# Kernel optimization log

Measured on AMD Instinct MI355X. Metric: run time of the kernel, lower is better.

The kernel has to match this reference:

```python
import jax, jax.numpy as jnp
import numpy as np

M_SQRT1_2 = 0.7071067811865476
P_DROP = 0.1  # activation_dropout


def setup_inputs() -> dict:
    key = jax.random.key(0)
    k1, k2, k3, k4 = jax.random.split(key, 4)
    N, FFN, EMB = 8192, 4096, 1024
    x = jax.random.normal(k1, (N, FFN), dtype=jnp.float16)
    weight = (jax.random.normal(k2, (EMB, FFN), dtype=jnp.float32) * (1.0 / np.sqrt(FFN))).astype(jnp.float16)
    bias = jax.random.normal(k3, (EMB,), dtype=jnp.float16)
    mask = jax.random.uniform(k4, (N, FFN)) >= P_DROP  # keep mask (bool)
    return {"x": x, "weight": weight, "bias": bias, "mask": mask}


def reference(x, weight, bias, mask):
    # GELU computed in fp32, cast back to fp16 (matches the custom IR)
    xf = x.astype(jnp.float32)
    g = (0.5 * xf * (1.0 + jax.lax.erf(xf * M_SQRT1_2))).astype(jnp.float16)
    # dropout: mask then scale by 1/(1-p) in fp16
    scale = jnp.float16(1.0 / (1.0 - P_DROP))
    h = g * mask.astype(jnp.float16) * scale  # [N, FFN]
    # y[N0, N2] = sum_N1 h[N0, N1] * weight[N2, N1] + bias[N2]
    y = jnp.einsum('nf,ef->ne', h, weight) + bias[None, :]
    return y
```

## Files before the change

kernel.cpp:

```cpp
#include <hip/hip_runtime.h>
#include <stdint.h>

typedef uint32_t u32;
typedef uint16_t u16;

static constexpr int M_DIM = 8192;
static constexpr int N_DIM = 1024;
static constexpr int K_DIM = 4096;

static constexpr int BM = 256;
static constexpr int BN = 128;
static constexpr int BK = 64;
static constexpr int KT64 = K_DIM / BK;
static constexpr int K_TILES32 = K_DIM / 32;
static constexpr int MB_TILES = M_DIM / 16;
static constexpr int NB_TILES = N_DIM / 16;

static constexpr size_t FRAG_U16 = 512;
static constexpr size_t HT_BYTES = (size_t)MB_TILES * K_TILES32 * FRAG_U16 * 2;
static constexpr size_t WT_BYTES = (size_t)NB_TILES * K_TILES32 * FRAG_U16 * 2;
static constexpr size_t WS_NEEDED = HT_BYTES + WT_BYTES;

typedef __attribute__((ext_vector_type(8))) _Float16 half8;
typedef __attribute__((ext_vector_type(4))) float f32x4;

__device__ __forceinline__ u32 pack2(float a, float b) {
  union { _Float16 h[2]; u32 u; } p;
  p.h[0] = (_Float16)a;
  p.h[1] = (_Float16)b;
  return p.u;
}

__device__ __forceinline__ float gelu_drop(float x, u32 keep) {
  float ax = fabsf(x);
  float z  = ax * 0.70710678f;
  float t  = __builtin_amdgcn_rcpf(fmaf(0.3275911f, z, 1.0f));
  float poly = fmaf(fmaf(fmaf(fmaf(1.061405429f, t, -1.453152027f),
                              t, 1.421413741f),
                         t, -0.284496736f),
                    t, 0.254829592f) * t;
  float e   = exp2f(z * z * -1.44269504f);
  float erf = fmaf(-poly, e, 1.0f);
  float g   = 0.5f * x * (1.0f + copysignf(erf, x));
  return keep ? g * 1.1111112f : 0.0f;
}

__device__ __forceinline__ void async_cp16(const void* g, void* l) {
  __builtin_amdgcn_global_load_lds((__attribute__((address_space(1))) u32*)g,
                                   (__attribute__((address_space(3))) u32*)l,
                                   16, 0, 0);
}

static constexpr int H_PAIRS = MB_TILES * (K_TILES32 / 2);
static constexpr int W_PAIRS = NB_TILES * (K_TILES32 / 2);
static constexpr int PACK_BLOCKS = (H_PAIRS + W_PAIRS) / 4;

__global__ __launch_bounds__(256)
void pack_kernel(const float* __restrict__ X, const int* __restrict__ Mask,
                 const float* __restrict__ W, u16* __restrict__ Ht, u16* __restrict__ Wt) {
  const int l     = threadIdx.x & 63;
  const int pi    = blockIdx.x * 4 + (threadIdx.x >> 6);
  const int row16 = l & 15;
  const int kof   = (l >> 4) << 4;

  const int fsub = kof >> 5;
  const int q0   = (kof & 31) >> 3;

  if (pi < H_PAIRS) {
    const int mb = pi >> 6, kp = pi & 63;
    const size_t src = (size_t)(mb * 16 + row16) * K_DIM + kp * 64 + kof;
    const float* xp = X    + src;
    const int*   mp = Mask + src;
    float4 x0 = *(const float4*)(xp + 0);
    float4 x1 = *(const float4*)(xp + 4);
    float4 x2 = *(const float4*)(xp + 8);
    float4 x3 = *(const float4*)(xp + 12);
    uint4  m0 = *(const uint4*)(mp + 0);
    uint4  m1 = *(const uint4*)(mp + 4);
    uint4  m2 = *(const uint4*)(mp + 8);
    uint4  m3 = *(const uint4*)(mp + 12);
    u32 o0 = pack2(gelu_drop(x0.x, m0.x), gelu_drop(x0.y, m0.y));
    u32 o1 = pack2(gelu_drop(x0.z, m0.z), gelu_drop(x0.w, m0.w));
    u32 o2 = pack2(gelu_drop(x1.x, m1.x), gelu_drop(x1.y, m1.y));
    u32 o3 = pack2(gelu_drop(x1.z, m1.z), gelu_drop(x1.w, m1.w));
    u32 o4 = pack2(gelu_drop(x2.x, m2.x), gelu_drop(x2.y, m2.y));
    u32 o5 = pack2(gelu_drop(x2.z, m2.z), gelu_drop(x2.w, m2.w));
    u32 o6 = pack2(gelu_drop(x3.x, m3.x), gelu_drop(x3.y, m3.y));
    u32 o7 = pack2(gelu_drop(x3.z, m3.z), gelu_drop(x3.w, m3.w));
    const int f = kp * 2 + fsub;
    u16* dst = Ht + (size_t)(mb * 128 + f) * FRAG_U16 + (size_t)(row16 + 16 * q0) * 8;
    *(uint4*)(dst)       = make_uint4(o0, o1, o2, o3);
    *(uint4*)(dst + 128) = make_uint4(o4, o5, o6, o7);
  } else {
    const int pj = pi - H_PAIRS;
    const int nb = pj >> 6, kp = pj & 63;
    const float* wp = W + (size_t)(nb * 16 + row16) * K_DIM + kp * 64 + kof;
    float4 w0 = *(const float4*)(wp + 0);
    float4 w1 = *(const float4*)(wp + 4);
    float4 w2 = *(const float4*)(wp + 8);
    float4 w3 = *(const float4*)(wp + 12);
    const int f = kp * 2 + fsub;
    u16* dst = Wt + (size_t)(nb * 128 + f) * FRAG_U16 + (size_t)(row16 + 16 * q0) * 8;
    *(uint4*)(dst)       = make_uint4(pack2(w0.x, w0.y), pack2(w0.z, w0.w),
                                      pack2(w1.x, w1.y), pack2(w1.z, w1.w));
    *(uint4*)(dst + 128) = make_uint4(pack2(w2.x, w2.y), pack2(w2.z, w2.w),
                                      pack2(w3.x, w3.y), pack2(w3.z, w3.w));
  }
}

__global__ __launch_bounds__(512, 1)
void gemm_kernel(const u16* __restrict__ Ht, const u16* __restrict__ Wt,
                 const float* __restrict__ Bias, float* __restrict__ Out) {
  __shared__ __attribute__((aligned(16))) u16 Abuf[3][BM * BK];
  __shared__ __attribute__((aligned(16))) u16 Bbuf[3][BN * BK];

  const int tid  = threadIdx.x;
  const int lane = tid & 63;
  const int wv   = tid >> 6;
  const int wr   = wv >> 1;
  const int wc   = wv & 1;

  const int bm = blockIdx.x & 31;
  const int bn = blockIdx.x >> 5;
  const int m0 = bm * BM;
  const int n0 = bn * BN;

  const char* aG = (const char*)Ht;
  const char* bG = (const char*)Wt;
  size_t aOff[4], bOff[2];
#pragma unroll
  for (int p = 0; p < 4; ++p) {
    const int s = tid + 512 * p, f = s >> 6;
    aOff[p] = ((size_t)(bm * 16 + (f >> 1)) * K_TILES32 + (f & 1)) * 1024 + (size_t)(s & 63) * 16;
  }
#pragma unroll
  for (int p = 0; p < 2; ++p) {
    const int s = tid + 512 * p, f = s >> 6;
    bOff[p] = ((size_t)(bn * 8 + (f >> 1)) * K_TILES32 + (f & 1)) * 1024 + (size_t)(s & 63) * 16;
  }

  auto stageHalf = [&](int kt, int buf, int h) {
    const size_t ko = (size_t)kt * 2048;
    char* ad = (char*)Abuf[buf];
    char* bd = (char*)Bbuf[buf];
    if (h == 0) {
      async_cp16(aG + aOff[0] + ko, ad + (size_t)(tid)*16);
      async_cp16(aG + aOff[1] + ko, ad + (size_t)(tid + 512) * 16);
      async_cp16(bG + bOff[0] + ko, bd + (size_t)(tid)*16);
    } else {
      async_cp16(aG + aOff[2] + ko, ad + (size_t)(tid + 1024) * 16);
      async_cp16(aG + aOff[3] + ko, ad + (size_t)(tid + 1536) * 16);
      async_cp16(bG + bOff[1] + ko, bd + (size_t)(tid + 512) * 16);
    }
  };

  auto stageFull = [&](int kt, int buf) {
    stageHalf(kt, buf, 0);
    stageHalf(kt, buf, 1);
  };

  f32x4 acc[4][4];
#pragma unroll
  for (int i = 0; i < 4; ++i)
#pragma unroll
    for (int j = 0; j < 4; ++j)
      acc[i][j] = (f32x4){0.f, 0.f, 0.f, 0.f};

  auto phase = [&](int buf, int kk, int stKt, int stBuf, int h, int vm) {
    const char* ab = (const char*)Abuf[buf];
    const char* bb = (const char*)Bbuf[buf];
    half8 ar[4], br[4];
#pragma unroll
    for (int i = 0; i < 4; ++i)
      ar[i] = *(const half8*)(ab + (size_t)(((wr * 4 + i) * 2 + kk) * 64 + lane) * 16);
#pragma unroll
    for (int j = 0; j < 4; ++j)
      br[j] = *(const half8*)(bb + (size_t)(((wc * 4 + j) * 2 + kk) * 64 + lane) * 16);
    if (stKt >= 0) stageHalf(stKt, stBuf, h);
    if (vm == 6) asm volatile("s_waitcnt vmcnt(6)" ::: "memory");
    else if (vm == 0) asm volatile("s_waitcnt vmcnt(0)" ::: "memory");
    __builtin_amdgcn_s_barrier();
    asm volatile("s_waitcnt lgkmcnt(0)" ::: "memory");
    __builtin_amdgcn_sched_barrier(0);
    __builtin_amdgcn_s_setprio(1);
#pragma unroll
    for (int i = 0; i < 4; ++i)
#pragma unroll
      for (int j = 0; j < 4; ++j)
        acc[i][j] = __builtin_amdgcn_mfma_f32_16x16x32_f16(ar[i], br[j], acc[i][j], 0, 0, 0);
    __builtin_amdgcn_s_setprio(0);
    __builtin_amdgcn_sched_barrier(0);
    __builtin_amdgcn_s_barrier();
  };

  stageFull(0, 0);
  stageFull(1, 1);
  asm volatile("s_waitcnt vmcnt(6)" ::: "memory");
  __builtin_amdgcn_s_barrier();

#pragma unroll 1
  for (int kt = 0; kt < KT64; ++kt) {
    const int cur  = kt % 3;
    const bool st  = (kt + 2) < KT64;
    const int  sb  = (kt + 2) % 3;
    const int vm = st ? 6 : ((kt + 1) < KT64 ? 0 : -1);
    phase(cur, 0, st ? kt + 2 : -1, sb, 0, -1);
    phase(cur, 1, st ? kt + 2 : -1, sb, 1, vm);
  }

  const int fr = lane & 15;
  const int rq = (lane >> 4) << 2;
  float bv[4];
#pragma unroll
  for (int j = 0; j < 4; ++j)
    bv[j] = Bias[n0 + wc * 64 + j * 16 + fr];

#pragma unroll
  for (int i = 0; i < 4; ++i) {
    const int row0 = m0 + wr * 64 + i * 16 + rq;
#pragma unroll
    for (int j = 0; j < 4; ++j) {
      const int col = n0 + wc * 64 + j * 16 + fr;
#pragma unroll
      for (int r = 0; r < 4; ++r)
        Out[(size_t)(row0 + r) * N_DIM + col] = acc[i][j][r] + bv[j];
    }
  }
}

static constexpr int A_STRIDE = 40;

__global__ __launch_bounds__(256, 2)
void fused_fallback_kernel(const float* __restrict__ X, const float* __restrict__ W,
                           const float* __restrict__ Bias, const int* __restrict__ Mask,
                           float* __restrict__ Out) {
  __shared__ __attribute__((aligned(16))) _Float16 As[128 * A_STRIDE];
  __shared__ __attribute__((aligned(16))) _Float16 Bs[128 * 32];

  const int tid  = threadIdx.x;
  const int lane = tid & 63;
  const int wv   = tid >> 6;
  const int wr   = wv >> 1;
  const int wc   = wv & 1;
  const int bm = blockIdx.x & 63;
  const int bn = blockIdx.x >> 6;
  const int m0 = bm * 128;
  const int n0 = bn * 128;

  const int a_m = tid >> 1;
  const int a_k = (tid & 1) << 4;
  const float* xptr = X    + (size_t)(m0 + a_m) * K_DIM + a_k;
  const int*   mptr = Mask + (size_t)(m0 + a_m) * K_DIM + a_k;
  _Float16* a_lds = &As[a_m * A_STRIDE + a_k];

  const int i0 = tid, i1 = tid + 256;
  const float* wp0 = W + (size_t)(n0 + (i0 >> 2)) * K_DIM + ((i0 & 3) << 3);
  const float* wp1 = W + (size_t)(n0 + (i1 >> 2)) * K_DIM + ((i1 & 3) << 3);
  _Float16* bl0 = &Bs[i0 * 8];
  _Float16* bl1 = &Bs[i1 * 8];

  f32x4 acc[4][4];
#pragma unroll
  for (int i = 0; i < 4; ++i)
#pragma unroll
    for (int j = 0; j < 4; ++j)
      acc[i][j] = (f32x4){0.f, 0.f, 0.f, 0.f};

  float4 xf0 = *(const float4*)(xptr +  0);
  float4 xf1 = *(const float4*)(xptr +  4);
  float4 xf2 = *(const float4*)(xptr +  8);
  float4 xf3 = *(const float4*)(xptr + 12);
  uint4  mr0 = *(const uint4*)(mptr +  0);
  uint4  mr1 = *(const uint4*)(mptr +  4);
  uint4  mr2 = *(const uint4*)(mptr +  8);
  uint4  mr3 = *(const uint4*)(mptr + 12);
  float4 wf0 = *(const float4*)(wp0 + 0);
  float4 wf1 = *(const float4*)(wp0 + 4);
  float4 wf2 = *(const float4*)(wp1 + 0);
  float4 wf3 = *(const float4*)(wp1 + 4);

#pragma unroll 1
  for (int kt = 0; kt < 128; ++kt) {
    {
      float xs[16] = {xf0.x, xf0.y, xf0.z, xf0.w, xf1.x, xf1.y, xf1.z, xf1.w,
                      xf2.x, xf2.y, xf2.z, xf2.w, xf3.x, xf3.y, xf3.z, xf3.w};
      u32 mk[16]   = {mr0.x, mr0.y, mr0.z, mr0.w, mr1.x, mr1.y, mr1.z, mr1.w,
                      mr2.x, mr2.y, mr2.z, mr2.w, mr3.x, mr3.y, mr3.z, mr3.w};
      u32 ow[8];
#pragma unroll
      for (int e = 0; e < 8; ++e)
        ow[e] = pack2(gelu_drop(xs[2 * e], mk[2 * e]), gelu_drop(xs[2 * e + 1], mk[2 * e + 1]));
      ((uint4*)a_lds)[0] = make_uint4(ow[0], ow[1], ow[2], ow[3]);
      ((uint4*)a_lds)[1] = make_uint4(ow[4], ow[5], ow[6], ow[7]);
    }
    {
      *(uint4*)bl0 = make_uint4(pack2(wf0.x, wf0.y), pack2(wf0.z, wf0.w),
                                pack2(wf1.x, wf1.y), pack2(wf1.z, wf1.w));
      *(uint4*)bl1 = make_uint4(pack2(wf2.x, wf2.y), pack2(wf2.z, wf2.w),
                                pack2(wf3.x, wf3.y), pack2(wf3.z, wf3.w));
    }
    __syncthreads();

    if (kt + 1 < 128) {
      xptr += 32; mptr += 32; wp0 += 32; wp1 += 32;
      xf0 = *(const float4*)(xptr +  0);
      xf1 = *(const float4*)(xptr +  4);
      xf2 = *(const float4*)(xptr +  8);
      xf3 = *(const float4*)(xptr + 12);
      mr0 = *(const uint4*)(mptr +  0);
      mr1 = *(const uint4*)(mptr +  4);
      mr2 = *(const uint4*)(mptr +  8);
      mr3 = *(const uint4*)(mptr + 12);
      wf0 = *(const float4*)(wp0 + 0);
      wf1 = *(const float4*)(wp0 + 4);
      wf2 = *(const float4*)(wp1 + 0);
      wf3 = *(const float4*)(wp1 + 4);
    }

    {
      const int fr2 = lane & 15;
      const int fk2 = (lane >> 4) << 3;
      half8 ar[4], br[4];
#pragma unroll
      for (int i = 0; i < 4; ++i)
        ar[i] = *(const half8*)&As[(wr * 64 + i * 16 + fr2) * A_STRIDE + fk2];
#pragma unroll
      for (int j = 0; j < 4; ++j)
        br[j] = *(const half8*)&Bs[(wc * 64 + j * 16 + fr2) * 32 + fk2];
#pragma unroll
      for (int i = 0; i < 4; ++i)
#pragma unroll
        for (int j = 0; j < 4; ++j)
          acc[i][j] = __builtin_amdgcn_mfma_f32_16x16x32_f16(ar[i], br[j], acc[i][j], 0, 0, 0);
    }
    __syncthreads();
  }

  const int fr = lane & 15;
  const int rq = (lane >> 4) << 2;
  float bv[4];
#pragma unroll
  for (int j = 0; j < 4; ++j)
    bv[j] = Bias[n0 + wc * 64 + j * 16 + fr];
#pragma unroll
  for (int i = 0; i < 4; ++i) {
    const int row0 = m0 + wr * 64 + i * 16 + rq;
#pragma unroll
    for (int j = 0; j < 4; ++j) {
      const int col = n0 + wc * 64 + j * 16 + fr;
#pragma unroll
      for (int r = 0; r < 4; ++r)
        Out[(size_t)(row0 + r) * N_DIM + col] = acc[i][j][r] + bv[j];
    }
  }
}

extern "C" void kernel_launch(void* const* d_in, const int* in_sizes, int n_in,
                              void* d_out, int out_size, void* d_ws, size_t ws_size,
                              hipStream_t stream) {
  const float* X    = (const float*)d_in[0];
  const float* W    = (const float*)d_in[1];
  const float* Bias = (const float*)d_in[2];
  const int*   Mk   = (const int*)d_in[3];
  float* Out = (float*)d_out;

  if (ws_size >= WS_NEEDED) {
    u16* Ht = (u16*)d_ws;
    u16* Wt = (u16*)((char*)d_ws + HT_BYTES);
    pack_kernel<<<PACK_BLOCKS, 256, 0, stream>>>(X, Mk, W, Ht, Wt);
    gemm_kernel<<<(M_DIM / BM) * (N_DIM / BN), 512, 0, stream>>>(Ht, Wt, Bias, Out);
  } else {
    fused_fallback_kernel<<<64 * 8, 256, 0, stream>>>(X, W, Bias, Mk, Out);
  }
}
```

Baseline: 389.0 us.

## Fuse GELU-dropout into GEMM with full-N row tiles and streamed weights

Drops the separate pass that packed the activated input to workspace. GELU and dropout are now computed inside the GEMM: each block loads a 32-row slice of X and the mask, activates it, and writes it into swizzled LDS double buffers. Each block covers all 1024 output columns, while pre-packed fp16 weight fragments stream through a triple-buffered async LDS pipeline. This removes the fp16 H write and re-read, but every block re-streams the whole weight matrix (relying on L2), and each block does far less MFMA work per LDS B load.

```diff
diff --git a/kernel.cpp b/kernel.cpp
--- a/kernel.cpp
+++ b/kernel.cpp
@@ -8,18 +8,9 @@
 static constexpr int N_DIM = 1024;
 static constexpr int K_DIM = 4096;
 
-static constexpr int BM = 256;
-static constexpr int BN = 128;
-static constexpr int BK = 64;
-static constexpr int KT64 = K_DIM / BK;
-static constexpr int K_TILES32 = K_DIM / 32;
-static constexpr int MB_TILES = M_DIM / 16;
-static constexpr int NB_TILES = N_DIM / 16;
-
 static constexpr size_t FRAG_U16 = 512;
-static constexpr size_t HT_BYTES = (size_t)MB_TILES * K_TILES32 * FRAG_U16 * 2;
-static constexpr size_t WT_BYTES = (size_t)NB_TILES * K_TILES32 * FRAG_U16 * 2;
-static constexpr size_t WS_NEEDED = HT_BYTES + WT_BYTES;
+static constexpr size_t WT_BYTES = 64ull * 128 * FRAG_U16 * 2;
+static constexpr size_t WS_NEEDED = WT_BYTES;
 
 typedef __attribute__((ext_vector_type(8))) _Float16 half8;
 typedef __attribute__((ext_vector_type(4))) float f32x4;
@@ -51,179 +42,180 @@
                                    16, 0, 0);
 }
 
-static constexpr int H_PAIRS = MB_TILES * (K_TILES32 / 2);
-static constexpr int W_PAIRS = NB_TILES * (K_TILES32 / 2);
-static constexpr int PACK_BLOCKS = (H_PAIRS + W_PAIRS) / 4;
+__device__ __forceinline__ u32 aswz(u32 b) {
+  return b ^ (((b >> 8) & 3u) << 4) ^ (((b >> 10) & 1u) << 6);
+}
+
+static constexpr int W_PAIRS = 64 * 64;
+static constexpr int WPACK_BLOCKS = W_PAIRS / 4;
 
 __global__ __launch_bounds__(256)
-void pack_kernel(const float* __restrict__ X, const int* __restrict__ Mask,
-                 const float* __restrict__ W, u16* __restrict__ Ht, u16* __restrict__ Wt) {
+void wpack_kernel(const float* __restrict__ W, u16* __restrict__ Wt) {
   const int l     = threadIdx.x & 63;
-  const int pi    = blockIdx.x * 4 + (threadIdx.x >> 6);
+  const int pj    = blockIdx.x * 4 + (threadIdx.x >> 6);
   const int row16 = l & 15;
   const int kof   = (l >> 4) << 4;
-
-  const int fsub = kof >> 5;
-  const int q0   = (kof & 31) >> 3;
-
-  if (pi < H_PAIRS) {
-    const int mb = pi >> 6, kp = pi & 63;
-    const size_t src = (size_t)(mb * 16 + row16) * K_DIM + kp * 64 + kof;
-    const float* xp = X    + src;
-    const int*   mp = Mask + src;
-    float4 x0 = *(const float4*)(xp + 0);
-    float4 x1 = *(const float4*)(xp + 4);
-    float4 x2 = *(const float4*)(xp + 8);
-    float4 x3 = *(const float4*)(xp + 12);
-    uint4  m0 = *(const uint4*)(mp + 0);
-    uint4  m1 = *(const uint4*)(mp + 4);
-    uint4  m2 = *(const uint4*)(mp + 8);
-    uint4  m3 = *(const uint4*)(mp + 12);
-    u32 o0 = pack2(gelu_drop(x0.x, m0.x), gelu_drop(x0.y, m0.y));
-    u32 o1 = pack2(gelu_drop(x0.z, m0.z), gelu_drop(x0.w, m0.w));
-    u32 o2 = pack2(gelu_drop(x1.x, m1.x), gelu_drop(x1.y, m1.y));
-    u32 o3 = pack2(gelu_drop(x1.z, m1.z), gelu_drop(x1.w, m1.w));
-    u32 o4 = pack2(gelu_drop(x2.x, m2.x), gelu_drop(x2.y, m2.y));
-    u32 o5 = pack2(gelu_drop(x2.z, m2.z), gelu_drop(x2.w, m2.w));
-    u32 o6 = pack2(gelu_drop(x3.x, m3.x), gelu_drop(x3.y, m3.y));
-    u32 o7 = pack2(gelu_drop(x3.z, m3.z), gelu_drop(x3.w, m3.w));
-    const int f = kp * 2 + fsub;
-    u16* dst = Ht + (size_t)(mb * 128 + f) * FRAG_U16 + (size_t)(row16 + 16 * q0) * 8;
-    *(uint4*)(dst)       = make_uint4(o0, o1, o2, o3);
-    *(uint4*)(dst + 128) = make_uint4(o4, o5, o6, o7);
-  } else {
-    const int pj = pi - H_PAIRS;
-    const int nb = pj >> 6, kp = pj & 63;
-    const float* wp = W + (size_t)(nb * 16 + row16) * K_DIM + kp * 64 + kof;
-    float4 w0 = *(const float4*)(wp + 0);
-    float4 w1 = *(const float4*)(wp + 4);
-    float4 w2 = *(const float4*)(wp + 8);
-    float4 w3 = *(const float4*)(wp + 12);
-    const int f = kp * 2 + fsub;
-    u16* dst = Wt + (size_t)(nb * 128 + f) * FRAG_U16 + (size_t)(row16 + 16 * q0) * 8;
-    *(uint4*)(dst)       = make_uint4(pack2(w0.x, w0.y), pack2(w0.z, w0.w),
-                                      pack2(w1.x, w1.y), pack2(w1.z, w1.w));
-    *(uint4*)(dst + 128) = make_uint4(pack2(w2.x, w2.y), pack2(w2.z, w2.w),
-                                      pack2(w3.x, w3.y), pack2(w3.z, w3.w));
-  }
+  const int fsub  = kof >> 5;
+  const int q0    = (kof & 31) >> 3;
+
+  const int nb = pj >> 6, kp = pj & 63;
+  const float* wp = W + (size_t)(nb * 16 + row16) * K_DIM + kp * 64 + kof;
+  float4 w0 = *(const float4*)(wp + 0);
+  float4 w1 = *(const float4*)(wp + 4);
+  float4 w2 = *(const float4*)(wp + 8);
+  float4 w3 = *(const float4*)(wp + 12);
+  const int f = kp * 2 + fsub;
+  u16* dst = Wt + (size_t)(nb * 128 + f) * FRAG_U16 + (size_t)(row16 + 16 * q0) * 8;
+  *(uint4*)(dst)       = make_uint4(pack2(w0.x, w0.y), pack2(w0.z, w0.w),
+                                    pack2(w1.x, w1.y), pack2(w1.z, w1.w));
+  *(uint4*)(dst + 128) = make_uint4(pack2(w2.x, w2.y), pack2(w2.z, w2.w),
+                                    pack2(w3.x, w3.y), pack2(w3.z, w3.w));
 }
 
 __global__ __launch_bounds__(512, 1)
-void gemm_kernel(const u16* __restrict__ Ht, const u16* __restrict__ Wt,
-                 const float* __restrict__ Bias, float* __restrict__ Out) {
-  __shared__ __attribute__((aligned(16))) u16 Abuf[3][BM * BK];
-  __shared__ __attribute__((aligned(16))) u16 Bbuf[3][BN * BK];
+void fused_gemm_kernel(const float* __restrict__ X, const int* __restrict__ Mask,
+                       const u16* __restrict__ Wt, const float* __restrict__ Bias,
+                       float* __restrict__ Out) {
+  __shared__ __attribute__((aligned(16))) u16 Bbuf[3 * 16384];
+  __shared__ __attribute__((aligned(16))) u16 Abuf[2 * 4096];
 
   const int tid  = threadIdx.x;
   const int lane = tid & 63;
   const int wv   = tid >> 6;
-  const int wr   = wv >> 1;
-  const int wc   = wv & 1;
-
-  const int bm = blockIdx.x & 31;
-  const int bn = blockIdx.x >> 5;
-  const int m0 = bm * BM;
-  const int n0 = bn * BN;
-
-  const char* aG = (const char*)Ht;
-  const char* bG = (const char*)Wt;
-  size_t aOff[4], bOff[2];
-#pragma unroll
-  for (int p = 0; p < 4; ++p) {
-    const int s = tid + 512 * p, f = s >> 6;
-    aOff[p] = ((size_t)(bm * 16 + (f >> 1)) * K_TILES32 + (f & 1)) * 1024 + (size_t)(s & 63) * 16;
-  }
-#pragma unroll
-  for (int p = 0; p < 2; ++p) {
-    const int s = tid + 512 * p, f = s >> 6;
-    bOff[p] = ((size_t)(bn * 8 + (f >> 1)) * K_TILES32 + (f & 1)) * 1024 + (size_t)(s & 63) * 16;
-  }
-
-  auto stageHalf = [&](int kt, int buf, int h) {
-    const size_t ko = (size_t)kt * 2048;
-    char* ad = (char*)Abuf[buf];
-    char* bd = (char*)Bbuf[buf];
-    if (h == 0) {
-      async_cp16(aG + aOff[0] + ko, ad + (size_t)(tid)*16);
-      async_cp16(aG + aOff[1] + ko, ad + (size_t)(tid + 512) * 16);
-      async_cp16(bG + bOff[0] + ko, bd + (size_t)(tid)*16);
-    } else {
-      async_cp16(aG + aOff[2] + ko, ad + (size_t)(tid + 1024) * 16);
-      async_cp16(aG + aOff[3] + ko, ad + (size_t)(tid + 1536) * 16);
-      async_cp16(bG + bOff[1] + ko, bd + (size_t)(tid + 512) * 16);
-    }
-  };
-
-  auto stageFull = [&](int kt, int buf) {
-    stageHalf(kt, buf, 0);
-    stageHalf(kt, buf, 1);
-  };
-
-  f32x4 acc[4][4];
-#pragma unroll
-  for (int i = 0; i < 4; ++i)
-#pragma unroll
-    for (int j = 0; j < 4; ++j)
+  const int m0   = blockIdx.x * 32;
+
+  char* Bb = (char*)Bbuf;
+  char* Ab = (char*)Abuf;
+  const char* WtB = (const char*)Wt;
+
+  u32 fOff[4];
+#pragma unroll
+  for (int p2 = 0; p2 < 4; ++p2) {
+    const int s = tid + 512 * p2;
+    fOff[p2] = (u32)((s >> 6) * 131072 + (s & 63) * 16);
+  }
+  auto stageB = [&](int kt, int h, int slot) {
+#pragma unroll
+    for (int p2 = 0; p2 < 4; ++p2)
+      async_cp16(WtB + (size_t)h * 4194304 + fOff[p2] + (size_t)kt * 1024,
+                 Bb + (size_t)slot * 32768 + (size_t)(tid + 512 * p2) * 16);
+  };
+
+  const int xrow = tid >> 4;
+  const int xe   = tid & 15;
+  const float* Xp = X    + (size_t)(m0 + xrow) * K_DIM + xe * 8;
+  const int*   Mp = Mask + (size_t)(m0 + xrow) * K_DIM + xe * 8;
+  float4 xs0, xs1;
+  uint4  ms0, ms1;
+  auto loadX = [&](int c) {
+    const float* xp = Xp + c * 128;
+    const int*   mp = Mp + c * 128;
+    xs0 = *(const float4*)(xp);
+    xs1 = *(const float4*)(xp + 4);
+    ms0 = *(const uint4*)(mp);
+    ms1 = *(const uint4*)(mp + 4);
+  };
+
+  const u32 aWbase = (u32)(((((u32)xrow >> 4) << 2) | ((u32)xe >> 2)) * 1024 +
+                           ((u32)xe & 3) * 256 + ((u32)xrow & 15) * 16);
+  auto writeA = [&](int aslot) {
+    u32 o0 = pack2(gelu_drop(xs0.x, ms0.x), gelu_drop(xs0.y, ms0.y));
+    u32 o1 = pack2(gelu_drop(xs0.z, ms0.z), gelu_drop(xs0.w, ms0.w));
+    u32 o2 = pack2(gelu_drop(xs1.x, ms1.x), gelu_drop(xs1.y, ms1.y));
+    u32 o3 = pack2(gelu_drop(xs1.z, ms1.z), gelu_drop(xs1.w, ms1.w));
+    *(uint4*)(Ab + aslot * 8192 + aswz(aWbase)) = make_uint4(o0, o1, o2, o3);
+  };
+
+  f32x4 acc[2][8];
+#pragma unroll
+  for (int i = 0; i < 2; ++i)
+#pragma unroll
+    for (int j = 0; j < 8; ++j)
       acc[i][j] = (f32x4){0.f, 0.f, 0.f, 0.f};
 
-  auto phase = [&](int buf, int kk, int stKt, int stBuf, int h, int vm) {
-    const char* ab = (const char*)Abuf[buf];
-    const char* bb = (const char*)Bbuf[buf];
-    half8 ar[4], br[4];
-#pragma unroll
-    for (int i = 0; i < 4; ++i)
-      ar[i] = *(const half8*)(ab + (size_t)(((wr * 4 + i) * 2 + kk) * 64 + lane) * 16);
-#pragma unroll
-    for (int j = 0; j < 4; ++j)
-      br[j] = *(const half8*)(bb + (size_t)(((wc * 4 + j) * 2 + kk) * 64 + lane) * 16);
-    if (stKt >= 0) stageHalf(stKt, stBuf, h);
-    if (vm == 6) asm volatile("s_waitcnt vmcnt(6)" ::: "memory");
-    else if (vm == 0) asm volatile("s_waitcnt vmcnt(0)" ::: "memory");
-    __builtin_amdgcn_s_barrier();
+  const u32 bRdBase = (u32)(wv * 4096 + lane * 16);
+
+  half8 arK[2];
+  auto readA = [&](int aslot, int ktl) {
+#pragma unroll
+    for (int rf = 0; rf < 2; ++rf) {
+      u32 b = (u32)(((rf << 2) | ktl) * 1024 + lane * 16);
+      arK[rf] = *(const half8*)(Ab + aslot * 8192 + aswz(b));
+    }
+  };
+  auto mfmaPhase = [&](int rdslot, int h) {
+    half8 br[4];
+#pragma unroll
+    for (int jj = 0; jj < 4; ++jj)
+      br[jj] = *(const half8*)(Bb + (size_t)rdslot * 32768 + bRdBase + jj * 1024);
     asm volatile("s_waitcnt lgkmcnt(0)" ::: "memory");
     __builtin_amdgcn_sched_barrier(0);
     __builtin_amdgcn_s_setprio(1);
 #pragma unroll
-    for (int i = 0; i < 4; ++i)
-#pragma unroll
-      for (int j = 0; j < 4; ++j)
-        acc[i][j] = __builtin_amdgcn_mfma_f32_16x16x32_f16(ar[i], br[j], acc[i][j], 0, 0, 0);
+    for (int rf = 0; rf < 2; ++rf)
+#pragma unroll
+      for (int jj = 0; jj < 4; ++jj)
+        acc[rf][h * 4 + jj] =
+            __builtin_amdgcn_mfma_f32_16x16x32_f16(arK[rf], br[jj], acc[rf][h * 4 + jj], 0, 0, 0);
     __builtin_amdgcn_s_setprio(0);
     __builtin_amdgcn_sched_barrier(0);
-    __builtin_amdgcn_s_barrier();
-  };
-
-  stageFull(0, 0);
-  stageFull(1, 1);
-  asm volatile("s_waitcnt vmcnt(6)" ::: "memory");
+  };
+
+  loadX(0);
+  stageB(0, 0, 0);
+  stageB(0, 1, 1);
+  writeA(0);
+  asm volatile("s_waitcnt vmcnt(4)" ::: "memory");
+  asm volatile("s_waitcnt lgkmcnt(0)" ::: "memory");
   __builtin_amdgcn_s_barrier();
 
+  int rdslot = 0, stslot = 2;
 #pragma unroll 1
-  for (int kt = 0; kt < KT64; ++kt) {
-    const int cur  = kt % 3;
-    const bool st  = (kt + 2) < KT64;
-    const int  sb  = (kt + 2) % 3;
-    const int vm = st ? 6 : ((kt + 1) < KT64 ? 0 : -1);
-    phase(cur, 0, st ? kt + 2 : -1, sb, 0, -1);
-    phase(cur, 1, st ? kt + 2 : -1, sb, 1, vm);
+  for (int c = 0; c < 32; ++c) {
+    const int aslot = c & 1;
+#pragma unroll
+    for (int ktl = 0; ktl < 4; ++ktl) {
+      const int kt = c * 4 + ktl;
+      if (ktl == 0 && c + 1 < 32) loadX(c + 1);
+      if (kt < 127) stageB(kt + 1, 0, stslot);
+      readA(aslot, ktl);
+      mfmaPhase(rdslot, 0);
+      if (ktl == 1 && c + 1 < 32) writeA(aslot ^ 1);
+      if (kt < 127) {
+        if (ktl == 0 && c + 1 < 32) { asm volatile("s_waitcnt vmcnt(8)" ::: "memory"); }
+        else                        { asm volatile("s_waitcnt vmcnt(4)" ::: "memory"); }
+      } else {
+        asm volatile("s_waitcnt vmcnt(0)" ::: "memory");
+      }
+      asm volatile("s_waitcnt lgkmcnt(0)" ::: "memory");
+      __builtin_amdgcn_s_barrier();
+      rdslot = (rdslot == 2) ? 0 : rdslot + 1;
+      stslot = (stslot == 2) ? 0 : stslot + 1;
+      if (kt < 127) stageB(kt + 1, 1, stslot);
+      mfmaPhase(rdslot, 1);
+      if (kt < 127) {
+        asm volatile("s_waitcnt vmcnt(4)" ::: "memory");
+        asm volatile("s_waitcnt lgkmcnt(0)" ::: "memory");
+        __builtin_amdgcn_s_barrier();
+        rdslot = (rdslot == 2) ? 0 : rdslot + 1;
+        stslot = (stslot == 2) ? 0 : stslot + 1;
+      }
+    }
   }
 
   const int fr = lane & 15;
   const int rq = (lane >> 4) << 2;
-  float bv[4];
-#pragma unroll
-  for (int j = 0; j < 4; ++j)
-    bv[j] = Bias[n0 + wc * 64 + j * 16 + fr];
-
-#pragma unroll
-  for (int i = 0; i < 4; ++i) {
-    const int row0 = m0 + wr * 64 + i * 16 + rq;
-#pragma unroll
-    for (int j = 0; j < 4; ++j) {
-      const int col = n0 + wc * 64 + j * 16 + fr;
+#pragma unroll
+  for (int rf = 0; rf < 2; ++rf) {
+    const int row0 = m0 + rf * 16 + rq;
+#pragma unroll
+    for (int j = 0; j < 8; ++j) {
+      const int nb16 = (j < 4) ? (wv * 4 + j) : (32 + wv * 4 + (j - 4));
+      const int col = nb16 * 16 + fr;
+      const float b = Bias[col];
 #pragma unroll
       for (int r = 0; r < 4; ++r)
-        Out[(size_t)(row0 + r) * N_DIM + col] = acc[i][j][r] + bv[j];
+        Out[(size_t)(row0 + r) * N_DIM + col] = acc[rf][j][r] + b;
     }
   }
 }
@@ -365,10 +357,9 @@
   float* Out = (float*)d_out;
 
   if (ws_size >= WS_NEEDED) {
-    u16* Ht = (u16*)d_ws;
-    u16* Wt = (u16*)((char*)d_ws + HT_BYTES);
-    pack_kernel<<<PACK_BLOCKS, 256, 0, stream>>>(X, Mk, W, Ht, Wt);
-    gemm_kernel<<<(M_DIM / BM) * (N_DIM / BN), 512, 0, stream>>>(Ht, Wt, Bias, Out);
+    u16* Wt = (u16*)d_ws;
+    wpack_kernel<<<WPACK_BLOCKS, 256, 0, stream>>>(W, Wt);
+    fused_gemm_kernel<<<M_DIM / 32, 512, 0, stream>>>(X, Mk, Wt, Bias, Out);
   } else {
     fused_fallback_kernel<<<64 * 8, 256, 0, stream>>>(X, W, Bias, Mk, Out);
   }
```

Result: slower. 479.4 us (+23.2%).
